# Optimization experiments

Measured on AMD Instinct MI355X. Metric: run time of the kernel, lower is better.

## Reference

```python
import jax, jax.numpy as jnp
import numpy as np

EPS = 1e-5

def adain_norm(x):
    # per-(batch,channel) instance normalization over spatial dims (AdaIN projection)
    mean = jnp.mean(x, axis=(2, 3), keepdims=True)
    var = jnp.var(x, axis=(2, 3), keepdims=True)
    return (x - mean) / jnp.sqrt(var + EPS)

def conv1x1(x, w, b):
    # x: [B,C,H,W], w: [O,C], b: [O]
    return jnp.einsum('bchw,oc->bohw', x, w) + b[None, :, None, None]

def setup_inputs() -> dict:
    key = jax.random.key(0)
    ks = jax.random.split(key, 10)
    B, C, H, W = 4, 512, 64, 64
    s = 1.0 / np.sqrt(C)
    return {
        'x': jax.random.normal(ks[0], (B, C, H, W), jnp.float32),
        'y': jax.random.normal(ks[1], (B, C, H, W), jnp.float32),
        'f_w': jax.random.normal(ks[2], (C, C), jnp.float32) * s,
        'f_b': jnp.zeros((C,), jnp.float32),
        'g_w': jax.random.normal(ks[3], (C, C), jnp.float32) * s,
        'g_b': jnp.zeros((C,), jnp.float32),
        'h_w': jax.random.normal(ks[4], (C, C), jnp.float32) * s,
        'h_b': jnp.zeros((C,), jnp.float32),
        'out_w': jax.random.normal(ks[5], (C, C), jnp.float32) * s,
        'out_b': jnp.zeros((C,), jnp.float32),
    }

def reference(x, y, f_w, f_b, g_w, g_b, h_w, h_b, out_w, out_b):
    B, C, H, W = x.shape
    HW = H * W
    xn = adain_norm(x)
    yn = adain_norm(y)
    # 1x1 conv projections, flattened over spatial dims
    f = conv1x1(xn, f_w, f_b).reshape(B, C, HW)   # [B,C,HWx]
    g = conv1x1(yn, g_w, g_b).reshape(B, C, HW)   # [B,C,HWy]
    energy = jnp.einsum('bci,bcj->bij', f, g)     # [B,HWx,HWy]
    correlation = jax.nn.softmax(energy, axis=-1)
    h = conv1x1(y, h_w, h_b).reshape(B, C, HW)    # [B,C,HWy]
    # residual = h @ correlation^T -> [B,C,HWx]
    residual = jnp.einsum('bcj,bij->bci', h, correlation).reshape(B, C, H, W)
    residual = conv1x1(residual, out_w, out_b)
    return x + residual
```

## Files before the change

kernel.cpp:

```cpp
#include <hip/hip_runtime.h>
#include <stdint.h>

#define HW 4096
#define NC 512
#define NB 4

typedef __attribute__((ext_vector_type(8))) _Float16 f16x8;
typedef __attribute__((ext_vector_type(4))) float f32x4;
typedef __attribute__((ext_vector_type(4))) unsigned short ush4;
typedef __attribute__((ext_vector_type(8))) unsigned short ush8;

typedef __attribute__((address_space(1))) const void* as1_cvp;
typedef __attribute__((address_space(3))) void* as3_vp;

__device__ __forceinline__ unsigned short f2h(float f) {
  union { _Float16 h; unsigned short u; } c;
  c.h = (_Float16)f;
  return c.u;
}
__device__ __forceinline__ float h2f(unsigned short u) {
  union { unsigned short u; _Float16 h; } c;
  c.u = u;
  return (float)c.h;
}

__global__ __launch_bounds__(256) void moments_k(const float* __restrict__ x,
                                                 const float* __restrict__ y,
                                                 float* __restrict__ stats) {
  int bid = blockIdx.x;
  int tens = bid >> 11;
  int row = bid & 2047;
  const float* src = (tens ? y : x) + (size_t)row * HW;
  float s = 0.f, s2 = 0.f;
  for (int j = threadIdx.x; j < HW / 4; j += 256) {
    float4 v = ((const float4*)src)[j];
    s += (v.x + v.y) + (v.z + v.w);
    s2 += (v.x * v.x + v.y * v.y) + (v.z * v.z + v.w * v.w);
  }
  #pragma unroll
  for (int o = 32; o; o >>= 1) { s += __shfl_down(s, o); s2 += __shfl_down(s2, o); }
  __shared__ float rs[8];
  int w = threadIdx.x >> 6;
  if ((threadIdx.x & 63) == 0) { rs[w] = s; rs[4 + w] = s2; }
  __syncthreads();
  if (threadIdx.x == 0) {
    float S = (rs[0] + rs[1]) + (rs[2] + rs[3]);
    float S2 = (rs[4] + rs[5]) + (rs[6] + rs[7]);
    float mean = S * (1.f / HW);
    float var = S2 * (1.f / HW) - mean * mean;
    stats[tens * 4096 + row] = mean;
    stats[tens * 4096 + 2048 + row] = rsqrtf(var + 1e-5f);
  }
}

__global__ __launch_bounds__(256) void transnorm_k(const float* __restrict__ x,
                                                   const float* __restrict__ y,
                                                   const float* __restrict__ stats,
                                                   unsigned short* __restrict__ xnT,
                                                   unsigned short* __restrict__ ynT,
                                                   unsigned short* __restrict__ yT) {
  __shared__ float tile[64][65];
  __shared__ float ms[64], rsd[64];
  int zi = blockIdx.z;
  int b = zi >> 1, mode = zi & 1;
  int i0 = blockIdx.x * 64, c0 = blockIdx.y * 64;
  const float* src = mode ? y : x;
  int t = threadIdx.x;
  int c = t >> 2;
  int isub = (t & 3) << 4;
  if (t < 64) {
    int srow = (mode ? 4096 : 0) + b * NC + c0 + t;
    ms[t] = stats[srow];
    rsd[t] = stats[srow + 2048];
  }
  const float4* sp = (const float4*)(src + ((size_t)(b * NC + c0 + c)) * HW + i0 + isub);
  #pragma unroll
  for (int k = 0; k < 4; ++k) {
    float4 v = sp[k];
    int ib = isub + k * 4;
    tile[ib + 0][c] = v.x;
    tile[ib + 1][c] = v.y;
    tile[ib + 2][c] = v.z;
    tile[ib + 3][c] = v.w;
  }
  __syncthreads();
  int i = t >> 2;
  int cc = (t & 3) << 4;
  size_t obase = ((size_t)b * HW + i0 + i) * NC + c0 + cc;
  if (mode == 0) {
    #pragma unroll
    for (int h = 0; h < 2; ++h) {
      ush8 o;
      #pragma unroll
      for (int e = 0; e < 8; ++e) {
        int ce = cc + h * 8 + e;
        o[e] = f2h((tile[i][ce] - ms[ce]) * rsd[ce]);
      }
      *(ush8*)(xnT + obase + h * 8) = o;
    }
  } else {
    #pragma unroll
    for (int h = 0; h < 2; ++h) {
      ush8 on,or_;
      #pragma unroll
      for (int e = 0; e < 8; ++e) {
        int ce = cc + h * 8 + e;
        float raw = tile[i][ce];
        on[e] = f2h((raw - ms[ce]) * rsd[ce]);
        or_[e] = f2h(raw);
      }
      *(ush8*)(ynT + obase + h * 8) = on;
      *(ush8*)(yT + obase + h * 8) = or_;
    }
  }
}

__global__ __launch_bounds__(256) void castw_k(const float* __restrict__ fw,
                                               const float* __restrict__ gw,
                                               const float* __restrict__ hw_,
                                               const float* __restrict__ ow,
                                               unsigned short* __restrict__ dst) {
  int idx = blockIdx.x * 256 + threadIdx.x;
  int which = idx >> 16;
  int sub = idx & 65535;
  const float* s = which == 0 ? fw : which == 1 ? gw : which == 2 ? hw_ : ow;
  float4 v = ((const float4*)s)[sub];
  ush4 o;
  o[0] = f2h(v.x); o[1] = f2h(v.y); o[2] = f2h(v.z); o[3] = f2h(v.w);
  *(ush4*)(dst + (size_t)idx * 4) = o;
}

__global__ __launch_bounds__(256) void softmax_h(unsigned short* __restrict__ S) {
  unsigned short* row = S + (size_t)blockIdx.x * HW;
  int t = threadIdx.x;
  ush8 a0 = *(const ush8*)(row + t * 16);
  ush8 a1 = *(const ush8*)(row + t * 16 + 8);
  float v[16];
  #pragma unroll
  for (int e = 0; e < 8; ++e) { v[e] = h2f(a0[e]); v[8 + e] = h2f(a1[e]); }
  float mx = -3.0e38f;
  #pragma unroll
  for (int e = 0; e < 16; ++e) mx = fmaxf(mx, v[e]);
  #pragma unroll
  for (int o = 32; o; o >>= 1) mx = fmaxf(mx, __shfl_down(mx, o));
  __shared__ float red[8];
  int w = t >> 6;
  if ((t & 63) == 0) red[w] = mx;
  __syncthreads();
  mx = fmaxf(fmaxf(red[0], red[1]), fmaxf(red[2], red[3]));
  float sum = 0.f;
  #pragma unroll
  for (int e = 0; e < 16; ++e) { v[e] = __expf(v[e] - mx); sum += v[e]; }
  #pragma unroll
  for (int o = 32; o; o >>= 1) sum += __shfl_down(sum, o);
  if ((t & 63) == 0) red[4 + w] = sum;
  __syncthreads();
  float inv = 1.f / ((red[4] + red[5]) + (red[6] + red[7]));
  ush8 o0, o1;
  #pragma unroll
  for (int e = 0; e < 8; ++e) { o0[e] = f2h(v[e] * inv); o1[e] = f2h(v[8 + e] * inv); }
  *(ush8*)(row + t * 16) = o0;
  *(ush8*)(row + t * 16 + 8) = o1;
}

__global__ __launch_bounds__(256) void reduce_k(const float* __restrict__ P4,
                                                unsigned short* __restrict__ op,
                                                long long PSo, int R, int pzs) {
  int e = blockIdx.x * 256 + threadIdx.x;
  int bg = e >> pzs;
  int rem = e - (bg << pzs);
  const float4* base = (const float4*)P4 + ((size_t)bg * 4) * R * (NC / 4) + rem;
  float4 s = {0.f, 0.f, 0.f, 0.f};
  #pragma unroll
  for (int sp = 0; sp < 4; ++sp) {
    float4 v = base[(size_t)sp * R * (NC / 4)];
    s.x += v.x; s.y += v.y; s.z += v.z; s.w += v.w;
  }
  int m = rem >> 7, c4 = rem & 127;
  ush4 o;
  o[0] = f2h(s.x); o[1] = f2h(s.y); o[2] = f2h(s.z); o[3] = f2h(s.w);
  *(ush4*)(op + (size_t)bg * PSo + (size_t)m * NC + c4 * 4) = o;
}

__global__ __launch_bounds__(256) void gemm_nt(
    const unsigned short* __restrict__ A, long long sA, int lda,
    const unsigned short* __restrict__ Bm, long long sB, int ldb,
    void* __restrict__ Cp, long long sC, long long sCs, int ldc,
    int K, int out_f32, int ls,
    const float* __restrict__ bias_m, const float* __restrict__ bias_n,
    const float* __restrict__ add_src, long long sAdd,
    const unsigned short* __restrict__ B2, const float* __restrict__ bias_n2,
    int zsw) {
  __shared__ short lsA[128 * 64];
  __shared__ short lsB[128 * 64];
  const int t = threadIdx.x;
  const int lane = t & 63;
  const int w = t >> 6;
  const int wm = w >> 1, wn = w & 1;
  const long long bz = blockIdx.z;
  if ((int)bz >= zsw) { Bm = B2; bias_n = bias_n2; }
  const long long bg = bz >> ls;
  const int sp = (int)(bz - (bg << ls));
  const long long koff = (long long)sp * K;
  const unsigned short* Ab = A + bz * sA * (ls ? 0 : 1) + (ls ? bg * sA : 0) + koff
                           + (size_t)blockIdx.x * 128 * lda;
  const unsigned short* Bb = Bm + bg * sB + koff + (size_t)blockIdx.y * 128 * ldb;

  f32x4 zero = {0.f, 0.f, 0.f, 0.f};
  f32x4 acc[4][4];
  #pragma unroll
  for (int i = 0; i < 4; ++i)
    #pragma unroll
    for (int j = 0; j < 4; ++j) acc[i][j] = zero;

  const int nkt = K >> 6;
  for (int kt = 0; kt < nkt; ++kt) {
    const int kbase = kt << 6;
    #pragma unroll
    for (int i = 0; i < 4; ++i) {
      int q = t + i * 256;
      int r = q >> 3, xx = q & 7;
      int gk = kbase + ((xx ^ (r & 7)) << 3);
      __builtin_amdgcn_global_load_lds((as1_cvp)(const void*)(Ab + (size_t)r * lda + gk),
                                       (as3_vp)(void*)(&lsA[q << 3]), 16, 0, 0);
      __builtin_amdgcn_global_load_lds((as1_cvp)(const void*)(Bb + (size_t)r * ldb + gk),
                                       (as3_vp)(void*)(&lsB[q << 3]), 16, 0, 0);
    }
    __syncthreads();
    #pragma unroll
    for (int ks = 0; ks < 2; ++ks) {
      f16x8 av[4], bv[4];
      const int xl = ks * 4 + (lane >> 4);
      const int rr = lane & 15;
      #pragma unroll
      for (int mb = 0; mb < 4; ++mb) {
        int row = wm * 64 + mb * 16 + rr;
        av[mb] = *(const f16x8*)&lsA[(row << 6) + ((xl ^ (row & 7)) << 3)];
      }
      #pragma unroll
      for (int nb = 0; nb < 4; ++nb) {
        int row = wn * 64 + nb * 16 + rr;
        bv[nb] = *(const f16x8*)&lsB[(row << 6) + ((xl ^ (row & 7)) << 3)];
      }
      #pragma unroll
      for (int mb = 0; mb < 4; ++mb)
        #pragma unroll
        for (int nb = 0; nb < 4; ++nb)
          acc[mb][nb] = __builtin_amdgcn_mfma_f32_16x16x32_f16(av[mb], bv[nb], acc[mb][nb], 0, 0, 0);
    }
    __syncthreads();
  }

  const int mb0 = blockIdx.x * 128 + wm * 64;
  const int nb0 = blockIdx.y * 128 + wn * 64;
  const int cn = lane & 15;
  const int rq = (lane >> 4) << 2;
  float* cf = (float*)Cp;
  unsigned short* ch = (unsigned short*)Cp;
  #pragma unroll
  for (int mb = 0; mb < 4; ++mb) {
    #pragma unroll
    for (int nb = 0; nb < 4; ++nb) {
      int n = nb0 + nb * 16 + cn;
      float bn = bias_n ? bias_n[n] : 0.f;
      #pragma unroll
      for (int r = 0; r < 4; ++r) {
        int m = mb0 + mb * 16 + rq + r;
        float vv = acc[mb][nb][r] + bn;
        if (bias_m) vv += bias_m[m];
        if (add_src) vv += add_src[bg * sAdd + (size_t)m * ldc + n];
        size_t off = (size_t)(bg * sC) + (size_t)sp * sCs + (size_t)m * ldc + n;
        if (out_f32) cf[off] = vv;
        else ch[off] = f2h(vv);
      }
    }
  }
}

__global__ __launch_bounds__(512, 2) void gemm_nt2(
    const unsigned short* __restrict__ A, long long sA, int lda,
    const unsigned short* __restrict__ Bm, long long sB, int ldb,
    void* __restrict__ Cp, long long sC, int ldc,
    int K, int out_f32) {
  __shared__ short lsA[2][256 * 64];
  __shared__ short lsB[2][256 * 64];
  const int t = threadIdx.x;
  const int lane = t & 63;
  const int w = t >> 6;
  const int wm = w >> 2, wn = w & 3;
  const long long bz = blockIdx.z;
  const unsigned short* Ab = A + bz * sA + (size_t)blockIdx.x * 256 * lda;
  const unsigned short* Bb = Bm + bz * sB + (size_t)blockIdx.y * 256 * ldb;

  f32x4 zero = {0.f, 0.f, 0.f, 0.f};
  f32x4 acc[8][4];
  #pragma unroll
  for (int i = 0; i < 8; ++i)
    #pragma unroll
    for (int j = 0; j < 4; ++j) acc[i][j] = zero;

  const int rr = lane & 15;
  const int xl = lane >> 4;
  const int nkt = K >> 6;

  auto STAGE = [&](int buf, int kt) {
    const int kbase = kt << 6;
    #pragma unroll
    for (int i = 0; i < 4; ++i) {
      int q = t + i * 512;
      int r = q >> 3, xx = q & 7;
      int gk = kbase + ((xx ^ (r & 7)) << 3);
      __builtin_amdgcn_global_load_lds((as1_cvp)(const void*)(Ab + (size_t)r * lda + gk),
                                       (as3_vp)(void*)(&lsA[buf][q << 3]), 16, 0, 0);
      __builtin_amdgcn_global_load_lds((as1_cvp)(const void*)(Bb + (size_t)r * ldb + gk),
                                       (as3_vp)(void*)(&lsB[buf][q << 3]), 16, 0, 0);
    }
  };

  STAGE(0, 0);
  __syncthreads();
  int cur = 0;
  for (int kt = 0; kt < nkt; ++kt) {
    if (kt + 1 < nkt) STAGE(cur ^ 1, kt + 1);
    #pragma unroll
    for (int ks = 0; ks < 2; ++ks) {
      f16x8 av[8], bv[4];
      const int cb = ks * 4 + xl;
      #pragma unroll
      for (int mb = 0; mb < 8; ++mb) {
        int row = wm * 128 + mb * 16 + rr;
        av[mb] = *(const f16x8*)&lsA[cur][(row << 6) + ((cb ^ (row & 7)) << 3)];
      }
      #pragma unroll
      for (int nb = 0; nb < 4; ++nb) {
        int row = wn * 64 + nb * 16 + rr;
        bv[nb] = *(const f16x8*)&lsB[cur][(row << 6) + ((cb ^ (row & 7)) << 3)];
      }
      __builtin_amdgcn_s_setprio(1);
      #pragma unroll
      for (int mb = 0; mb < 8; ++mb)
        #pragma unroll
        for (int nb = 0; nb < 4; ++nb)
          acc[mb][nb] = __builtin_amdgcn_mfma_f32_16x16x32_f16(av[mb], bv[nb], acc[mb][nb], 0, 0, 0);
      __builtin_amdgcn_s_setprio(0);
    }
    __syncthreads();
    cur ^= 1;
  }

  const int mb0 = blockIdx.x * 256 + wm * 128;
  const int nb0 = blockIdx.y * 256 + wn * 64;
  const int cn = lane & 15;
  const int rq = (lane >> 4) << 2;
  float* cf = (float*)Cp;
  unsigned short* ch = (unsigned short*)Cp;
  #pragma unroll
  for (int mb = 0; mb < 8; ++mb) {
    #pragma unroll
    for (int nb = 0; nb < 4; ++nb) {
      int n = nb0 + nb * 16 + cn;
      #pragma unroll
      for (int r = 0; r < 4; ++r) {
        int m = mb0 + mb * 16 + rq + r;
        float vv = acc[mb][nb][r];
        size_t off = (size_t)(bz * sC) + (size_t)m * ldc + n;
        if (out_f32) cf[off] = vv;
        else ch[off] = f2h(vv);
      }
    }
  }
}

extern "C" void kernel_launch(void* const* d_in, const int* in_sizes, int n_in,
                              void* d_out, int out_size, void* d_ws, size_t ws_size,
                              hipStream_t stream) {
  const float* x = (const float*)d_in[0];
  const float* y = (const float*)d_in[1];
  const float* f_w = (const float*)d_in[2];
  const float* f_b = (const float*)d_in[3];
  const float* g_w = (const float*)d_in[4];
  const float* g_b = (const float*)d_in[5];
  const float* h_w = (const float*)d_in[6];
  const float* h_b = (const float*)d_in[7];
  const float* out_w = (const float*)d_in[8];
  const float* out_b = (const float*)d_in[9];
  float* out = (float*)d_out;

  char* ws = (char*)d_ws;
  size_t off = 0;
  auto alloc = [&](size_t bytes) -> char* {
    char* p = ws + off;
    off += (bytes + 255) & ~(size_t)255;
    return p;
  };
  const size_t TN = (size_t)NB * HW * NC;
  float* stats = (float*)alloc(8192 * sizeof(float));
  unsigned short* wB = (unsigned short*)alloc((size_t)4 * 512 * 512 * 2);
  unsigned short* xnT = (unsigned short*)alloc(TN * 2);
  unsigned short* ynT = (unsigned short*)alloc(TN * 2);
  unsigned short* yT = (unsigned short*)alloc(TN * 2);
  unsigned short* fB = (unsigned short*)alloc(TN * 2);
  unsigned short* gB = (unsigned short*)alloc(TN * 2);
  unsigned short* hB = (unsigned short*)alloc(TN * 2);
  unsigned short* oB = xnT;
  size_t remain = ws_size > off ? ws_size - off : 0;
  const size_t SB = (size_t)HW * HW * 2 + (size_t)4 * HW * NC * 4;
  int G, R = HW;
  if (remain >= 4 * SB)      { G = 4; }
  else if (remain >= 2 * SB) { G = 2; }
  else if (remain >= SB)     { G = 1; }
  else {
    G = 1;
    while (R > 128 && (size_t)R * (HW * 2 + 16 * NC) > remain) R >>= 1;
  }
  unsigned short* Sh = (unsigned short*)alloc((size_t)G * R * HW * 2);
  float* P4 = (float*)alloc((size_t)G * 4 * R * NC * 4);
  if (off > ws_size) return;

  castw_k<<<dim3(1024), dim3(256), 0, stream>>>(f_w, g_w, h_w, out_w, wB);
  moments_k<<<dim3(4096), dim3(256), 0, stream>>>(x, y, stats);
  transnorm_k<<<dim3(64, 8, 8), dim3(256), 0, stream>>>(x, y, stats, xnT, ynT, yT);

  const long long PS = (long long)HW * NC;
  const int BIG = 1 << 30;
  gemm_nt<<<dim3(32, 4, 8), dim3(256), 0, stream>>>(
      xnT, PS, NC, wB, 0, NC, fB, PS, 0, NC, NC, 0, 0,
      nullptr, f_b, nullptr, 0, wB + 262144, g_b, 4);
  gemm_nt<<<dim3(4, 32, NB), dim3(256), 0, stream>>>(
      wB + 524288, 0, NC, yT, PS, NC, hB, PS, 0, HW, NC, 0, 0,
      h_b, nullptr, nullptr, 0, nullptr, nullptr, BIG);

  const int pzs = 31 - __builtin_clz((unsigned)(R * (NC / 4)));
  for (int b0 = 0; b0 < NB; b0 += G) {
    for (int r0 = 0; r0 < HW; r0 += R) {
      if (R >= 256) {
        gemm_nt2<<<dim3(R / 256, HW / 256, G), dim3(512), 0, stream>>>(
            fB + ((size_t)b0 * HW + r0) * NC, PS, NC,
            gB + (size_t)b0 * PS, PS, NC,
            Sh, (long long)R * HW, HW, NC, 0);
      } else {
        gemm_nt<<<dim3(R / 128, 32, G), dim3(256), 0, stream>>>(
            fB + ((size_t)b0 * HW + r0) * NC, PS, NC,
            gB + (size_t)b0 * PS, PS, NC,
            Sh, (long long)R * HW, 0, HW, NC, 0, 0,
            nullptr, nullptr, nullptr, 0, nullptr, nullptr, BIG);
      }
      softmax_h<<<dim3(G * R), dim3(256), 0, stream>>>(Sh);
      gemm_nt<<<dim3(R / 128, 4, G * 4), dim3(256), 0, stream>>>(
          Sh, (long long)R * HW, HW,
          hB + (size_t)b0 * NC * HW, (long long)NC * HW, HW,
          P4, (long long)4 * R * NC, (long long)R * NC, NC, HW / 4, 1, 2,
          nullptr, nullptr, nullptr, 0, nullptr, nullptr, BIG);
      reduce_k<<<dim3(G * R / 2), dim3(256), 0, stream>>>(
          P4, oB + ((size_t)b0 * HW + r0) * NC, PS, R, pzs);
    }
  }
  gemm_nt<<<dim3(4, 32, NB), dim3(256), 0, stream>>>(
      wB + 786432, 0, NC, oB, PS, NC,
      out, (long long)NC * HW, 0, HW, NC, 1, 0,
      out_b, nullptr, x, (long long)NC * HW, nullptr, nullptr, BIG);
}
```

Measured before the change: 445.6 us.

## Double-buffer LDS tiles in gemm_nt and raise MFMA wave priority

Converts the generic NT GEMM into a double-buffered version: the next K-tile is loaded into the alternate LDS buffer via global_load_lds while MFMAs run on the current one, which drops one barrier per iteration. It also raises wave priority around the MFMA block and sets a launch-bounds hint of 2 blocks. The aim is to hide global-load latency behind compute. The cost is doubled LDS use (64KB per block), which can cut occupancy, and the single remaining barrier has to cover both the reads of the current buffer and the completion of the async loads.

```diff
diff --git a/kernel.cpp b/kernel.cpp
--- a/kernel.cpp
+++ b/kernel.cpp
@@ -182,7 +182,7 @@
   *(ush4*)(op + (size_t)bg * PSo + (size_t)m * NC + c4 * 4) = o;
 }
 
-__global__ __launch_bounds__(256) void gemm_nt(
+__global__ __launch_bounds__(256, 2) void gemm_ntp(
     const unsigned short* __restrict__ A, long long sA, int lda,
     const unsigned short* __restrict__ Bm, long long sB, int ldb,
     void* __restrict__ Cp, long long sC, long long sCs, int ldc,
@@ -191,8 +191,8 @@
     const float* __restrict__ add_src, long long sAdd,
     const unsigned short* __restrict__ B2, const float* __restrict__ bias_n2,
     int zsw) {
-  __shared__ short lsA[128 * 64];
-  __shared__ short lsB[128 * 64];
+  __shared__ short lsA[2][128 * 64];
+  __shared__ short lsB[2][128 * 64];
   const int t = threadIdx.x;
   const int lane = t & 63;
   const int w = t >> 6;
@@ -214,7 +214,8 @@
     for (int j = 0; j < 4; ++j) acc[i][j] = zero;
 
   const int nkt = K >> 6;
-  for (int kt = 0; kt < nkt; ++kt) {
+
+  auto STAGE = [&](int buf, int kt) {
     const int kbase = kt << 6;
     #pragma unroll
     for (int i = 0; i < 4; ++i) {
@@ -222,11 +223,17 @@
       int r = q >> 3, xx = q & 7;
       int gk = kbase + ((xx ^ (r & 7)) << 3);
       __builtin_amdgcn_global_load_lds((as1_cvp)(const void*)(Ab + (size_t)r * lda + gk),
-                                       (as3_vp)(void*)(&lsA[q << 3]), 16, 0, 0);
+                                       (as3_vp)(void*)(&lsA[buf][q << 3]), 16, 0, 0);
       __builtin_amdgcn_global_load_lds((as1_cvp)(const void*)(Bb + (size_t)r * ldb + gk),
-                                       (as3_vp)(void*)(&lsB[q << 3]), 16, 0, 0);
-    }
-    __syncthreads();
+                                       (as3_vp)(void*)(&lsB[buf][q << 3]), 16, 0, 0);
+    }
+  };
+
+  STAGE(0, 0);
+  __syncthreads();
+  int cur = 0;
+  for (int kt = 0; kt < nkt; ++kt) {
+    if (kt + 1 < nkt) STAGE(cur ^ 1, kt + 1);
     #pragma unroll
     for (int ks = 0; ks < 2; ++ks) {
       f16x8 av[4], bv[4];
@@ -235,20 +242,23 @@
       #pragma unroll
       for (int mb = 0; mb < 4; ++mb) {
         int row = wm * 64 + mb * 16 + rr;
-        av[mb] = *(const f16x8*)&lsA[(row << 6) + ((xl ^ (row & 7)) << 3)];
+        av[mb] = *(const f16x8*)&lsA[cur][(row << 6) + ((xl ^ (row & 7)) << 3)];
       }
       #pragma unroll
       for (int nb = 0; nb < 4; ++nb) {
         int row = wn * 64 + nb * 16 + rr;
-        bv[nb] = *(const f16x8*)&lsB[(row << 6) + ((xl ^ (row & 7)) << 3)];
-      }
+        bv[nb] = *(const f16x8*)&lsB[cur][(row << 6) + ((xl ^ (row & 7)) << 3)];
+      }
+      __builtin_amdgcn_s_setprio(1);
       #pragma unroll
       for (int mb = 0; mb < 4; ++mb)
         #pragma unroll
         for (int nb = 0; nb < 4; ++nb)
           acc[mb][nb] = __builtin_amdgcn_mfma_f32_16x16x32_f16(av[mb], bv[nb], acc[mb][nb], 0, 0, 0);
+      __builtin_amdgcn_s_setprio(0);
     }
     __syncthreads();
+    cur ^= 1;
   }
 
   const int mb0 = blockIdx.x * 128 + wm * 64;
@@ -423,10 +433,10 @@
 
   const long long PS = (long long)HW * NC;
   const int BIG = 1 << 30;
-  gemm_nt<<<dim3(32, 4, 8), dim3(256), 0, stream>>>(
+  gemm_ntp<<<dim3(32, 4, 8), dim3(256), 0, stream>>>(
       xnT, PS, NC, wB, 0, NC, fB, PS, 0, NC, NC, 0, 0,
       nullptr, f_b, nullptr, 0, wB + 262144, g_b, 4);
-  gemm_nt<<<dim3(4, 32, NB), dim3(256), 0, stream>>>(
+  gemm_ntp<<<dim3(4, 32, NB), dim3(256), 0, stream>>>(
       wB + 524288, 0, NC, yT, PS, NC, hB, PS, 0, HW, NC, 0, 0,
       h_b, nullptr, nullptr, 0, nullptr, nullptr, BIG);
 
@@ -439,14 +449,14 @@
             gB + (size_t)b0 * PS, PS, NC,
             Sh, (long long)R * HW, HW, NC, 0);
       } else {
-        gemm_nt<<<dim3(R / 128, 32, G), dim3(256), 0, stream>>>(
+        gemm_ntp<<<dim3(R / 128, 32, G), dim3(256), 0, stream>>>(
             fB + ((size_t)b0 * HW + r0) * NC, PS, NC,
             gB + (size_t)b0 * PS, PS, NC,
             Sh, (long long)R * HW, 0, HW, NC, 0, 0,
             nullptr, nullptr, nullptr, 0, nullptr, nullptr, BIG);
       }
       softmax_h<<<dim3(G * R), dim3(256), 0, stream>>>(Sh);
-      gemm_nt<<<dim3(R / 128, 4, G * 4), dim3(256), 0, stream>>>(
+      gemm_ntp<<<dim3(R / 128, 4, G * 4), dim3(256), 0, stream>>>(
           Sh, (long long)R * HW, HW,
           hB + (size_t)b0 * NC * HW, (long long)NC * HW, HW,
           P4, (long long)4 * R * NC, (long long)R * NC, NC, HW / 4, 1, 2,
@@ -455,7 +465,7 @@
           P4, oB + ((size_t)b0 * HW + r0) * NC, PS, R, pzs);
     }
   }
-  gemm_nt<<<dim3(4, 32, NB), dim3(256), 0, stream>>>(
+  gemm_ntp<<<dim3(4, 32, NB), dim3(256), 0, stream>>>(
       wB + 786432, 0, NC, oB, PS, NC,
       out, (long long)NC * HW, 0, HW, NC, 1, 0,
       out_b, nullptr, x, (long long)NC * HW, nullptr, nullptr, BIG);
```

Result: faster. 407.5 us (-8.5%).
